# Optimization experiments

Hardware: AMD Instinct MI355X
Metric: run time of the kernel (lower is better)

## Reference

```python
import jax, jax.numpy as jnp
import numpy as np

HEAD = 128
BLOCK = 16
MAX_POS = 32768


def _rope_cache(dim=HEAD, base=10000.0, max_pos=MAX_POS):
    # Mirrors PrecomputedRotaryEmbedding: inv_freq/t in bf16, then cos/sin.
    inv = (1.0 / base ** (jnp.arange(0, dim, 2, dtype=jnp.float32) / dim)).astype(jnp.bfloat16)
    t = jnp.arange(max_pos, dtype=jnp.bfloat16)
    freqs = t[:, None] * inv[None, :]                      # [P, dim/2]
    emb = jnp.concatenate([freqs, freqs], axis=-1)         # [P, dim]
    return jnp.cos(emb).astype(jnp.float32), jnp.sin(emb).astype(jnp.float32)


def _rotary(x, cos, sin):
    # x: [B, H, D], cos/sin: [B, D]
    d2 = x.shape[-1] // 2
    rot = jnp.concatenate([-x[..., d2:], x[..., :d2]], axis=-1)
    return x * cos[:, None, :] + rot * sin[:, None, :]


def setup_inputs() -> dict:
    key = jax.random.key(0)
    ks = jax.random.split(key, 8)
    B, H, Hkv, D = 32, 32, 8, 128
    blocks_per_seq, bs = 128, BLOCK
    nblk = B * blocks_per_seq
    query = jax.random.normal(ks[0], (B, H, D), dtype=jnp.float32)
    k_new = jax.random.normal(ks[1], (B, Hkv, D), dtype=jnp.float32)
    v_new = jax.random.normal(ks[2], (B, Hkv, D), dtype=jnp.float32)
    k_cache = jax.random.normal(ks[3], (nblk, bs, Hkv, D), dtype=jnp.float32)
    v_cache = jax.random.normal(ks[4], (nblk, bs, Hkv, D), dtype=jnp.float32)
    block_table = jnp.arange(nblk, dtype=jnp.int32).reshape(B, blocks_per_seq)
    context_lens = jax.random.randint(ks[5], (B,), 1, 2048, dtype=jnp.int32)
    return {"query": query, "key": k_new, "value": v_new,
            "k_cache": k_cache, "v_cache": v_cache,
            "block_table": block_table, "context_lens": context_lens}


def reference(query, key, value, k_cache, v_cache, block_table, context_lens):
    B, H, D = query.shape
    Hkv = key.shape[1]
    nblk, bs, _, _ = k_cache.shape
    max_ctx = block_table.shape[1] * bs

    cos_c, sin_c = _rope_cache(dim=D)
    pos = context_lens.astype(jnp.int32)
    cos, sin = cos_c[pos], sin_c[pos]                      # [B, D]
    q = _rotary(query, cos, sin)                           # [B, H, D]
    k_new = _rotary(key, cos, sin)                         # [B, Hkv, D]

    # Scatter new k/v into the paged cache at slot of token (ctx - 1).
    last = pos - 1
    slot = block_table[jnp.arange(B), last // bs] * bs + last % bs  # [B]
    kf = k_cache.reshape(nblk * bs, Hkv, D).at[slot].set(k_new)
    vf = v_cache.reshape(nblk * bs, Hkv, D).at[slot].set(value)

    # Gather per-sequence KV via block table (irregular paged access).
    t = jnp.arange(max_ctx)
    idx = block_table[:, t // bs].astype(jnp.int32) * bs + (t % bs)[None, :].astype(jnp.int32)  # [B, L]
    idx = jnp.clip(idx, 0, nblk * bs - 1)
    K = kf[idx]                                            # [B, L, Hkv, D]
    V = vf[idx]

    scale = D ** -0.5
    g = H // Hkv
    qg = q.reshape(B, Hkv, g, D)
    scores = jnp.einsum('bkgd,blkd->bkgl', qg, K) * scale  # [B, Hkv, g, L]
    valid = t[None, :] < pos[:, None]                      # [B, L]
    scores = jnp.where(valid[:, None, None, :], scores, -1e30)
    p = jax.nn.softmax(scores, axis=-1)
    out = jnp.einsum('bkgl,blkd->bkgd', p, V)              # [B, Hkv, g, D]
    return out.reshape(B, H, D)
```

## Files before the change

### kernel.cpp

```cpp
#include <hip/hip_runtime.h>
#include <hip/hip_bf16.h>
#include <math.h>

#define NB 32
#define NH 32
#define HKV 8
#define GQ 4
#define DH 128
#define BS 16
#define BPS 128
#define NSPLIT 8
#define TILE 32
#define PART_STRIDE 520

__device__ __forceinline__ float bf16r(float x) {
    return __bfloat162float(__float2bfloat16(x));
}

__global__ void rope_kernel(const float* __restrict__ q,
                            const float* __restrict__ knew,
                            const int* __restrict__ bt,
                            const int* __restrict__ ctx,
                            float* __restrict__ q_rot,
                            float* __restrict__ k_rot,
                            int* __restrict__ slot)
{
    int b = blockIdx.x;
    int d = threadIdx.x;
    int pos = ctx[b];
    int i2 = d & 63;
    float e  = (float)i2 * (1.0f / 64.0f);
    float pf = (float)pow(10000.0, (double)e);
    float inv = bf16r(1.0f / pf);
    float tb  = bf16r((float)pos);
    float fr  = bf16r(tb * inv);
    float c   = bf16r(cosf(fr));
    float s   = bf16r(sinf(fr));

    const float* qb = q + (size_t)b * NH * DH;
    float* qo = q_rot + (size_t)b * NH * DH;
    #pragma unroll 4
    for (int h = 0; h < NH; ++h) {
        float x  = qb[h * DH + d];
        float xr = (d < 64) ? -qb[h * DH + d + 64] : qb[h * DH + d - 64];
        qo[h * DH + d] = x * c + xr * s;
    }
    const float* kb = knew + (size_t)b * HKV * DH;
    float* ko = k_rot + (size_t)b * HKV * DH;
    #pragma unroll
    for (int h = 0; h < HKV; ++h) {
        float x  = kb[h * DH + d];
        float xr = (d < 64) ? -kb[h * DH + d + 64] : kb[h * DH + d - 64];
        ko[h * DH + d] = x * c + xr * s;
    }
    if (d == 0) {
        int last = pos - 1;
        slot[b] = bt[b * BPS + (last >> 4)] * BS + (last & 15);
    }
}

__global__ __launch_bounds__(256) void attn_partial(
    const float* __restrict__ kc, const float* __restrict__ vc,
    const float* __restrict__ vnew,
    const int* __restrict__ bt, const int* __restrict__ ctx,
    const float* __restrict__ q_rot, const float* __restrict__ k_rot,
    const int* __restrict__ slot, float* __restrict__ part)
{
    __shared__ float q_lds[GQ][DH];
    __shared__ float k_lds[TILE][DH];
    __shared__ float v_lds[TILE][DH];
    __shared__ float p_lds[GQ][TILE];
    __shared__ int   row_src[TILE];
    __shared__ int   slot_l[NB];

    int tid = threadIdx.x;
    int bid = blockIdx.x;
    int sp  = bid & (NSPLIT - 1);
    int kvh = (bid / NSPLIT) & (HKV - 1);
    int b   = bid / (NSPLIT * HKV);

    int L = ctx[b];
    int chunk = (L + NSPLIT - 1) / NSPLIT;
    int start = sp * chunk;
    int end   = min(L, start + chunk);

    {
        const float* qs = q_rot + ((size_t)b * NH + kvh * GQ) * DH;
        ((float*)q_lds)[tid]       = qs[tid];
        ((float*)q_lds)[tid + 256] = qs[tid + 256];
        if (tid < NB) slot_l[tid] = slot[tid];
    }
    __syncthreads();

    int lane = tid & 63;
    int h    = tid >> 6;
    int l    = lane & 31;
    int half = lane >> 5;

    float  m_run = -INFINITY;
    float  s_run = 0.0f;
    float2 acc   = make_float2(0.f, 0.f);

    for (int t0 = start; t0 < end; t0 += TILE) {
        int n = min(TILE, end - t0);

        if (tid < TILE) {
            int o = 0;
            if (tid < n) {
                int t = t0 + tid;
                int flat = bt[b * BPS + (t >> 4)] * BS + (t & 15);
                o = flat;
                #pragma unroll
                for (int j = 0; j < NB; ++j)
                    if (flat == slot_l[j]) o = -(j + 1);
            }
            row_src[tid] = o;
        }
        __syncthreads();

        #pragma unroll
        for (int i = 0; i < 4; ++i) {
            int idx = tid + i * 256;
            int r = idx >> 5, c4 = idx & 31;
            if (r < n) {
                int o = row_src[r];
                const float4 *ks, *vs;
                if (o >= 0) {
                    size_t off = (size_t)o * (HKV * DH) + (size_t)kvh * DH;
                    ks = (const float4*)(kc + off);
                    vs = (const float4*)(vc + off);
                } else {
                    int j = -o - 1;
                    size_t off = ((size_t)j * HKV + kvh) * DH;
                    ks = (const float4*)(k_rot + off);
                    vs = (const float4*)(vnew + off);
                }
                int sc = c4 ^ (r & 31);
                *(float4*)&k_lds[r][sc * 4] = ks[c4];
                *(float4*)&v_lds[r][sc * 4] = vs[c4];
            }
        }
        __syncthreads();

        float s = 0.f;
        if (l < n) {
            const float4* qrow = (const float4*)q_lds[h];
            #pragma unroll
            for (int k = 0; k < 16; ++k) {
                int j = half * 16 + k;
                float4 a  = qrow[j];
                float4 bb = *(const float4*)&k_lds[l][(j ^ l) * 4];
                s += a.x * bb.x + a.y * bb.y + a.z * bb.z + a.w * bb.w;
            }
        }
        s += __shfl_xor(s, 32);
        s *= 0.08838834764831845f;

        float sm = (l < n) ? s : -INFINITY;
        float tm = sm;
        #pragma unroll
        for (int off = 16; off >= 1; off >>= 1)
            tm = fmaxf(tm, __shfl_xor(tm, off));
        float mnew = fmaxf(m_run, tm);
        float p  = (l < n) ? expf(s - mnew) : 0.f;
        float ts = p;
        #pragma unroll
        for (int off = 16; off >= 1; off >>= 1)
            ts += __shfl_xor(ts, off);
        float r = expf(m_run - mnew);
        s_run = s_run * r + ts;
        m_run = mnew;
        acc.x *= r; acc.y *= r;
        if (half == 0) p_lds[h][l] = p;
        __syncthreads();

        int jc = lane >> 1, sub = lane & 1;
        for (int ll = 0; ll < n; ++ll) {
            float pv = p_lds[h][ll];
            const float2 vv = *(const float2*)&v_lds[ll][((jc ^ ll) << 2) + sub * 2];
            acc.x += pv * vv.x;
            acc.y += pv * vv.y;
        }
        __syncthreads();
    }

    float* pp = part + (size_t)bid * PART_STRIDE + h * 130;
    if (lane == 0) { pp[0] = m_run; pp[1] = s_run; }
    *(float2*)&pp[2 + lane * 2] = acc;
}

__global__ void reduce_kernel(const float* __restrict__ part,
                              float* __restrict__ out)
{
    int blk = blockIdx.x;
    int d   = threadIdx.x;
    int b   = blk >> 5;
    int hq  = blk & 31;
    int kvh = hq >> 2;
    int g   = hq & 3;
    const float* base = part + ((size_t)(b * HKV + kvh) * NSPLIT) * PART_STRIDE + g * 130;

    float M = -INFINITY;
    #pragma unroll
    for (int s = 0; s < NSPLIT; ++s)
        M = fmaxf(M, base[(size_t)s * PART_STRIDE]);
    float S = 0.f, o = 0.f;
    #pragma unroll
    for (int s = 0; s < NSPLIT; ++s) {
        float ms = base[(size_t)s * PART_STRIDE];
        float f  = expf(ms - M);
        S += base[(size_t)s * PART_STRIDE + 1] * f;
        o += base[(size_t)s * PART_STRIDE + 2 + d] * f;
    }
    out[(size_t)blk * DH + d] = o / S;
}

extern "C" void kernel_launch(void* const* d_in, const int* in_sizes, int n_in,
                              void* d_out, int out_size, void* d_ws, size_t ws_size,
                              hipStream_t stream)
{
    const float* q    = (const float*)d_in[0];
    const float* knew = (const float*)d_in[1];
    const float* vnew = (const float*)d_in[2];
    const float* kc   = (const float*)d_in[3];
    const float* vc   = (const float*)d_in[4];
    const int*   bt   = (const int*)d_in[5];
    const int*   ctx  = (const int*)d_in[6];
    float* out = (float*)d_out;

    float* ws    = (float*)d_ws;
    float* q_rot = ws;
    float* k_rot = ws + 131072;
    int*   slot  = (int*)(ws + 131072 + 32768);
    float* part  = ws + 131072 + 32768 + 64;

    rope_kernel<<<NB, 128, 0, stream>>>(q, knew, bt, ctx, q_rot, k_rot, slot);
    attn_partial<<<NB * HKV * NSPLIT, 256, 0, stream>>>(
        kc, vc, vnew, bt, ctx, q_rot, k_rot, slot, part);
    reduce_kernel<<<NB * NH, 128, 0, stream>>>(part, out);
}
```

Before: 91.65 us.

## Precompute paged row indices and register-prefetch next KV tile

Adds a separate kernel that resolves every (batch, token) position into a flat cache row or a new-token slot ahead of time, which removes the per-tile block-table lookup and slot search from the attention kernel. The attention kernel now holds the next tile's K/V in registers while it computes the current tile, and it drops two barriers per iteration. This overlaps global loads with compute. The cost is an extra kernel launch, a 256KB index buffer, and higher register use. The removed barriers could race if the next tile's LDS write starts before the previous tile's PV loop has finished reading, although the loop-top sync still orders some of this.

```diff
diff --git a/kernel.cpp b/kernel.cpp
--- a/kernel.cpp
+++ b/kernel.cpp
@@ -9,6 +9,7 @@
 #define DH 128
 #define BS 16
 #define BPS 128
+#define MAXC 2048
 #define NSPLIT 8
 #define TILE 32
 #define PART_STRIDE 520
@@ -19,11 +20,9 @@
 
 __global__ void rope_kernel(const float* __restrict__ q,
                             const float* __restrict__ knew,
-                            const int* __restrict__ bt,
                             const int* __restrict__ ctx,
                             float* __restrict__ q_rot,
-                            float* __restrict__ k_rot,
-                            int* __restrict__ slot)
+                            float* __restrict__ k_rot)
 {
     int b = blockIdx.x;
     int d = threadIdx.x;
@@ -53,25 +52,41 @@
         float xr = (d < 64) ? -kb[h * DH + d + 64] : kb[h * DH + d - 64];
         ko[h * DH + d] = x * c + xr * s;
     }
-    if (d == 0) {
-        int last = pos - 1;
-        slot[b] = bt[b * BPS + (last >> 4)] * BS + (last & 15);
-    }
+}
+
+__global__ void rowidx_kernel(const int* __restrict__ bt,
+                              const int* __restrict__ ctx,
+                              int* __restrict__ rowidx)
+{
+    __shared__ int slot_l[NB];
+    int tid = threadIdx.x;
+    if (tid < NB) {
+        int last = ctx[tid] - 1;
+        slot_l[tid] = bt[tid * BPS + (last >> 4)] * BS + (last & 15);
+    }
+    __syncthreads();
+    int g = blockIdx.x * 256 + tid;
+    int b = g >> 11;
+    int t = g & (MAXC - 1);
+    int flat = bt[b * BPS + (t >> 4)] * BS + (t & 15);
+    int o = flat;
+    #pragma unroll
+    for (int j = 0; j < NB; ++j)
+        if (flat == slot_l[j]) o = -(j + 1);
+    rowidx[g] = o;
 }
 
 __global__ __launch_bounds__(256) void attn_partial(
     const float* __restrict__ kc, const float* __restrict__ vc,
     const float* __restrict__ vnew,
-    const int* __restrict__ bt, const int* __restrict__ ctx,
+    const int* __restrict__ ctx,
     const float* __restrict__ q_rot, const float* __restrict__ k_rot,
-    const int* __restrict__ slot, float* __restrict__ part)
+    const int* __restrict__ rowidx, float* __restrict__ part)
 {
     __shared__ float q_lds[GQ][DH];
     __shared__ float k_lds[TILE][DH];
     __shared__ float v_lds[TILE][DH];
     __shared__ float p_lds[GQ][TILE];
-    __shared__ int   row_src[TILE];
-    __shared__ int   slot_l[NB];
 
     int tid = threadIdx.x;
     int bid = blockIdx.x;
@@ -88,42 +103,65 @@
         const float* qs = q_rot + ((size_t)b * NH + kvh * GQ) * DH;
         ((float*)q_lds)[tid]       = qs[tid];
         ((float*)q_lds)[tid + 256] = qs[tid + 256];
-        if (tid < NB) slot_l[tid] = slot[tid];
-    }
-    __syncthreads();
+    }
 
     int lane = tid & 63;
     int h    = tid >> 6;
     int l    = lane & 31;
     int half = lane >> 5;
+    int rr   = tid >> 5;
+    int c4   = tid & 31;
 
     float  m_run = -INFINITY;
     float  s_run = 0.0f;
     float2 acc   = make_float2(0.f, 0.f);
 
+    float4 kreg[4], vreg[4];
+
+    #pragma unroll
+    for (int i = 0; i < 4; ++i) {
+        int r = rr + i * 8;
+        int t = start + r;
+        if (t < end) {
+            int o = rowidx[(b << 11) | t];
+            const float4 *ks, *vs;
+            if (o >= 0) {
+                size_t off = (size_t)o * (HKV * DH) + (size_t)kvh * DH;
+                ks = (const float4*)(kc + off);
+                vs = (const float4*)(vc + off);
+            } else {
+                int j = -o - 1;
+                size_t off = ((size_t)j * HKV + kvh) * DH;
+                ks = (const float4*)(k_rot + off);
+                vs = (const float4*)(vnew + off);
+            }
+            kreg[i] = ks[c4];
+            vreg[i] = vs[c4];
+        }
+    }
+    __syncthreads();
+
     for (int t0 = start; t0 < end; t0 += TILE) {
         int n = min(TILE, end - t0);
 
-        if (tid < TILE) {
-            int o = 0;
-            if (tid < n) {
-                int t = t0 + tid;
-                int flat = bt[b * BPS + (t >> 4)] * BS + (t & 15);
-                o = flat;
-                #pragma unroll
-                for (int j = 0; j < NB; ++j)
-                    if (flat == slot_l[j]) o = -(j + 1);
-            }
-            row_src[tid] = o;
+        #pragma unroll
+        for (int i = 0; i < 4; ++i) {
+            int r = rr + i * 8;
+            if (t0 + r < end) {
+                int sc = c4 ^ r;
+                *(float4*)&k_lds[r][sc * 4] = kreg[i];
+                *(float4*)&v_lds[r][sc * 4] = vreg[i];
+            }
         }
         __syncthreads();
 
+        int t1 = t0 + TILE;
         #pragma unroll
         for (int i = 0; i < 4; ++i) {
-            int idx = tid + i * 256;
-            int r = idx >> 5, c4 = idx & 31;
-            if (r < n) {
-                int o = row_src[r];
+            int r = rr + i * 8;
+            int t = t1 + r;
+            if (t < end) {
+                int o = rowidx[(b << 11) | t];
                 const float4 *ks, *vs;
                 if (o >= 0) {
                     size_t off = (size_t)o * (HKV * DH) + (size_t)kvh * DH;
@@ -135,12 +173,10 @@
                     ks = (const float4*)(k_rot + off);
                     vs = (const float4*)(vnew + off);
                 }
-                int sc = c4 ^ (r & 31);
-                *(float4*)&k_lds[r][sc * 4] = ks[c4];
-                *(float4*)&v_lds[r][sc * 4] = vs[c4];
-            }
-        }
-        __syncthreads();
+                kreg[i] = ks[c4];
+                vreg[i] = vs[c4];
+            }
+        }
 
         float s = 0.f;
         if (l < n) {
@@ -172,7 +208,6 @@
         m_run = mnew;
         acc.x *= r; acc.y *= r;
         if (half == 0) p_lds[h][l] = p;
-        __syncthreads();
 
         int jc = lane >> 1, sub = lane & 1;
         for (int ll = 0; ll < n; ++ll) {
@@ -228,14 +263,15 @@
     const int*   ctx  = (const int*)d_in[6];
     float* out = (float*)d_out;
 
-    float* ws    = (float*)d_ws;
-    float* q_rot = ws;
-    float* k_rot = ws + 131072;
-    int*   slot  = (int*)(ws + 131072 + 32768);
-    float* part  = ws + 131072 + 32768 + 64;
-
-    rope_kernel<<<NB, 128, 0, stream>>>(q, knew, bt, ctx, q_rot, k_rot, slot);
+    float* ws     = (float*)d_ws;
+    float* q_rot  = ws;
+    float* k_rot  = ws + 131072;
+    int*   rowidx = (int*)(ws + 131072 + 32768);
+    float* part   = ws + 131072 + 32768 + 65536;
+
+    rope_kernel<<<NB, 128, 0, stream>>>(q, knew, ctx, q_rot, k_rot);
+    rowidx_kernel<<<NB * MAXC / 256, 256, 0, stream>>>(bt, ctx, rowidx);
     attn_partial<<<NB * HKV * NSPLIT, 256, 0, stream>>>(
-        kc, vc, vnew, bt, ctx, q_rot, k_rot, slot, part);
+        kc, vc, vnew, ctx, q_rot, k_rot, rowidx, part);
     reduce_kernel<<<NB * NH, 128, 0, stream>>>(part, out);
 }
```

After: 171.0 us. +86.5%, slower.
